# Performance work log

Hardware: AMD Instinct MI355X
Metric: run time of the kernel (lower is better)

Reference implementation:

```python
import jax, jax.numpy as jnp
import numpy as np

B, N, NIN, NH, NOUT = 32, 64, 256, 256, 2
E = N * (N - 1)
BN_EPS = 1e-5


def _xavier(k, fan_in, fan_out):
    return jax.random.normal(k, (fan_in, fan_out), jnp.float32) * np.sqrt(2.0 / (fan_in + fan_out))


def _mlp_params(key, n_in, n_hid, n_out):
    k1, k2 = jax.random.split(key)
    return {
        'w1': _xavier(k1, n_in, n_hid), 'b1': jnp.full((n_hid,), 0.1, jnp.float32),
        'w2': _xavier(k2, n_hid, n_out), 'b2': jnp.full((n_out,), 0.1, jnp.float32),
        'g': jnp.ones((n_out,), jnp.float32), 'beta': jnp.zeros((n_out,), jnp.float32),
    }


def setup_inputs() -> dict:
    key = jax.random.key(0)
    ks = jax.random.split(key, 7)
    inputs = jax.random.normal(ks[0], (B, N, NIN), jnp.float32)
    # fully-connected directed graph w/o self loops: edge e = (send i, recv j), i != j
    idx = np.array([(i, j) for i in range(N) for j in range(N) if i != j], dtype=np.int64)
    rel_send = np.zeros((E, N), np.float32)
    rel_rec = np.zeros((E, N), np.float32)
    rel_send[np.arange(E), idx[:, 0]] = 1.0
    rel_rec[np.arange(E), idx[:, 1]] = 1.0
    out = {'inputs': inputs, 'rel_rec': jnp.asarray(rel_rec), 'rel_send': jnp.asarray(rel_send)}
    for name, (ni, nh, no), k in [('mlp1', (NIN, NH, NH), ks[1]),
                                  ('mlp2', (2 * NH, NH, NH), ks[2]),
                                  ('mlp3', (NH, NH, NH), ks[3]),
                                  ('mlp4', (3 * NH, NH, NH), ks[4])]:
        p = _mlp_params(k, ni, nh, no)
        for pk, pv in p.items():
            out[f'{name}_{pk}'] = pv
    out['fc_w'] = _xavier(ks[5], NH, NOUT)
    out['fc_b'] = jnp.full((NOUT,), 0.1, jnp.float32)
    return out


def _mlp(x, w1, b1, w2, b2, g, beta):
    # Linear -> ELU -> Linear -> ELU -> BatchNorm1d (training-mode batch stats, biased var)
    h = jax.nn.elu(x @ w1 + b1)
    h = jax.nn.elu(h @ w2 + b2)
    mean = h.mean(axis=(0, 1))
    var = h.var(axis=(0, 1))
    return (h - mean) * jax.lax.rsqrt(var + BN_EPS) * g + beta


def reference(inputs, rel_rec, rel_send,
              mlp1_w1, mlp1_b1, mlp1_w2, mlp1_b2, mlp1_g, mlp1_beta,
              mlp2_w1, mlp2_b1, mlp2_w2, mlp2_b2, mlp2_g, mlp2_beta,
              mlp3_w1, mlp3_b1, mlp3_w2, mlp3_b2, mlp3_g, mlp3_beta,
              mlp4_w1, mlp4_b1, mlp4_w2, mlp4_b2, mlp4_g, mlp4_beta,
              fc_w, fc_b):
    x = _mlp(inputs, mlp1_w1, mlp1_b1, mlp1_w2, mlp1_b2, mlp1_g, mlp1_beta)  # [B,N,NH]
    # node2edge: gather sender/receiver node features per edge
    s = jnp.einsum('en,bnh->beh', rel_send, x)
    r = jnp.einsum('en,bnh->beh', rel_rec, x)
    x = jnp.concatenate([s, r], axis=-1)  # [B,E,2*NH]
    x = _mlp(x, mlp2_w1, mlp2_b1, mlp2_w2, mlp2_b2, mlp2_g, mlp2_beta)
    x_skip = x
    # edge2node: scatter-sum incoming edges per node, normalized by N
    inc = jnp.einsum('en,beh->bnh', rel_rec, x) / N
    x = _mlp(inc, mlp3_w1, mlp3_b1, mlp3_w2, mlp3_b2, mlp3_g, mlp3_beta)
    s = jnp.einsum('en,bnh->beh', rel_send, x)
    r = jnp.einsum('en,bnh->beh', rel_rec, x)
    x = jnp.concatenate([s, r, x_skip], axis=-1)  # [B,E,3*NH]
    x = _mlp(x, mlp4_w1, mlp4_b1, mlp4_w2, mlp4_b2, mlp4_g, mlp4_beta)
    return x @ fc_w + fc_b  # [B,E,NOUT]
```

## Files before the change

kernel.cpp:

```cpp
#include <hip/hip_runtime.h>

typedef __bf16 bf16_t;
typedef __bf16 bf16x8 __attribute__((ext_vector_type(8)));
typedef float  f32x4  __attribute__((ext_vector_type(4)));

#define NB    64
#define EB    4032
#define BATCH 32
#define H     256
#define M_EDGE (BATCH*EB)
#define M_NODE (BATCH*NB)
#define T2    4
#define BN_EPS 1e-5f

__device__ __forceinline__ void load_lds16(const void* g, void* l) {
    __builtin_amdgcn_global_load_lds(
        (const __attribute__((address_space(1))) unsigned int*)g,
        (__attribute__((address_space(3))) unsigned int*)l, 16, 0, 0);
}
__device__ __forceinline__ float elu(float v) { return v > 0.f ? v : __expf(v) - 1.f; }

template<bool AF32>
__global__ __launch_bounds__(256, 3)
void fused_mlp(const void* __restrict__ A0v,
               const bf16_t* __restrict__ W1f, const float* __restrict__ b1,
               const bf16_t* __restrict__ W2f, const float* __restrict__ b2,
               bf16_t* __restrict__ out, float* __restrict__ stats)
{
    const int m0 = blockIdx.x * 64;
    const int tid = threadIdx.x, wave = tid >> 6, lane = tid & 63;
    const int l15 = lane & 15, quad = lane >> 4;
    const int row = tid >> 2;
    const int c0 = (tid & 3) * 64;

    __shared__ bf16_t h1s[64 * 264];
    __shared__ float  sred[512];

    sred[tid] = 0.f; sred[256 + tid] = 0.f;

    if (AF32) {
        const float* af = (const float*)A0v + (size_t)(m0 + row) * 256 + c0;
#pragma unroll
        for (int j = 0; j < 8; ++j) {
            float4 lo = *(const float4*)(af + j * 8);
            float4 hi = *(const float4*)(af + j * 8 + 4);
            bf16x8 v;
            v[0]=(bf16_t)lo.x; v[1]=(bf16_t)lo.y; v[2]=(bf16_t)lo.z; v[3]=(bf16_t)lo.w;
            v[4]=(bf16_t)hi.x; v[5]=(bf16_t)hi.y; v[6]=(bf16_t)hi.z; v[7]=(bf16_t)hi.w;
            *(bf16x8*)&h1s[row * 264 + c0 + j * 8] = v;
        }
    } else {
        const bf16_t* src = (const bf16_t*)A0v + (size_t)(m0 + row) * 256 + c0;
#pragma unroll
        for (int j = 0; j < 8; ++j)
            *(bf16x8*)&h1s[row * 264 + c0 + j * 8] = *(const bf16x8*)(src + j * 8);
    }

    const bf16_t* W1W = W1f + (size_t)wave * 16384;
    const bf16_t* W2W = W2f + (size_t)wave * 16384;

    bf16x8 bcur[4], bnxt[4];
#pragma unroll
    for (int u = 0; u < 4; ++u)
        bcur[u] = *(const bf16x8*)(W1W + u * 512 + lane * 8);
    __syncthreads();

    f32x4 acc[4][4];
#pragma unroll
    for (int a = 0; a < 4; ++a)
#pragma unroll
        for (int u = 0; u < 4; ++u) acc[a][u] = (f32x4){0.f, 0.f, 0.f, 0.f};

#pragma unroll
    for (int ks = 0; ks < 8; ++ks) {
        if (ks < 7) {
#pragma unroll
            for (int u = 0; u < 4; ++u)
                bnxt[u] = *(const bf16x8*)(W1W + (ks + 1) * 2048 + u * 512 + lane * 8);
        }
        bf16x8 afr[4];
#pragma unroll
        for (int a = 0; a < 4; ++a)
            afr[a] = *(const bf16x8*)&h1s[(a * 16 + l15) * 264 + ks * 32 + quad * 8];
#pragma unroll
        for (int a = 0; a < 4; ++a)
#pragma unroll
            for (int u = 0; u < 4; ++u)
                acc[a][u] = __builtin_amdgcn_mfma_f32_16x16x32_bf16(afr[a], bcur[u], acc[a][u], 0, 0, 0);
#pragma unroll
        for (int u = 0; u < 4; ++u) bcur[u] = bnxt[u];
    }

#pragma unroll
    for (int u = 0; u < 4; ++u)
        bcur[u] = *(const bf16x8*)(W2W + u * 512 + lane * 8);
    __syncthreads();

#pragma unroll
    for (int u = 0; u < 4; ++u) {
        int   col = wave * 64 + u * 16 + l15;
        float bv  = b1[col];
#pragma unroll
        for (int a = 0; a < 4; ++a)
#pragma unroll
            for (int r = 0; r < 4; ++r)
                h1s[(a * 16 + quad * 4 + r) * 264 + col] = (bf16_t)elu(acc[a][u][r] + bv);
    }
    __syncthreads();

#pragma unroll
    for (int a = 0; a < 4; ++a)
#pragma unroll
        for (int u = 0; u < 4; ++u) acc[a][u] = (f32x4){0.f, 0.f, 0.f, 0.f};
#pragma unroll
    for (int ks = 0; ks < 8; ++ks) {
        if (ks < 7) {
#pragma unroll
            for (int u = 0; u < 4; ++u)
                bnxt[u] = *(const bf16x8*)(W2W + (ks + 1) * 2048 + u * 512 + lane * 8);
        }
        bf16x8 afr[4];
#pragma unroll
        for (int a = 0; a < 4; ++a)
            afr[a] = *(const bf16x8*)&h1s[(a * 16 + l15) * 264 + ks * 32 + quad * 8];
#pragma unroll
        for (int a = 0; a < 4; ++a)
#pragma unroll
            for (int u = 0; u < 4; ++u)
                acc[a][u] = __builtin_amdgcn_mfma_f32_16x16x32_bf16(afr[a], bcur[u], acc[a][u], 0, 0, 0);
#pragma unroll
        for (int u = 0; u < 4; ++u) bcur[u] = bnxt[u];
    }
    __syncthreads();

#pragma unroll
    for (int u = 0; u < 4; ++u) {
        int   col = wave * 64 + u * 16 + l15;
        float bv  = b2[col];
        float s = 0.f, q = 0.f;
#pragma unroll
        for (int a = 0; a < 4; ++a)
#pragma unroll
            for (int r = 0; r < 4; ++r) {
                float v = elu(acc[a][u][r] + bv);
                h1s[(a * 16 + quad * 4 + r) * 264 + col] = (bf16_t)v;
                s += v; q += v * v;
            }
        s += __shfl_xor(s, 16); s += __shfl_xor(s, 32);
        q += __shfl_xor(q, 16); q += __shfl_xor(q, 32);
        if (quad == 0) { atomicAdd(&sred[col], s); atomicAdd(&sred[256 + col], q); }
    }
    __syncthreads();

#pragma unroll
    for (int p = 0; p < 8; ++p) {
        int idx = p * 256 + tid;
        int r = idx >> 5, ch = idx & 31;
        *(uint4*)&out[(size_t)(m0 + r) * H + ch * 8] = *(const uint4*)&h1s[r * 264 + ch * 8];
    }
    atomicAdd(&stats[tid],     sred[tid]);
    atomicAdd(&stats[H + tid], sred[256 + tid]);
}

__global__ __launch_bounds__(256)
void node_gemm(const bf16_t* __restrict__ A, const float* __restrict__ statsIn,
               const float* __restrict__ g, const float* __restrict__ beta, float Mcnt,
               const bf16_t* __restrict__ Wt, const float* __restrict__ bias,
               float* __restrict__ out)
{
    const int m0 = blockIdx.x * 64;
    const int nb = blockIdx.y * 256;
    const int tid = threadIdx.x, wave = tid >> 6, lane = tid & 63;
    const int l15 = lane & 15, quad = lane >> 4;
    const int row = tid >> 2;
    const int cx8 = (((tid & 3) ^ ((tid >> 3) & 3))) * 8;
    const int sl8 = (tid & 3) * 8;
    const int xq8 = (quad ^ ((l15 >> 1) & 3)) * 8;
    __shared__ bf16_t As[64 * 32];
    __shared__ bf16_t Bs[256 * 32];
    __shared__ float  ss[512];

    {
        float mean = statsIn[tid] / Mcnt;
        float var  = statsIn[256 + tid] / Mcnt - mean * mean;
        float scl  = g[tid] * rsqrtf(var + BN_EPS);
        ss[tid]       = scl;
        ss[256 + tid] = beta[tid] - mean * scl;
    }
    __syncthreads();

    f32x4 acc[4][4];
#pragma unroll
    for (int t = 0; t < 4; ++t)
#pragma unroll
        for (int u = 0; u < 4; ++u) acc[t][u] = (f32x4){0.f, 0.f, 0.f, 0.f};

    for (int k0 = 0; k0 < 256; k0 += 32) {
        {
            int kc = k0 + cx8;
            bf16x8 v = *(const bf16x8*)(A + (size_t)(m0 + row) * 256 + kc);
            bf16x8 w;
#pragma unroll
            for (int j = 0; j < 8; ++j)
                w[j] = (bf16_t)((float)v[j] * ss[kc + j] + ss[256 + kc + j]);
            *(bf16x8*)&As[row * 32 + sl8] = w;
        }
#pragma unroll
        for (int p = 0; p < 4; ++p)
            load_lds16(Wt + (size_t)(nb + p * 64 + row) * 256 + k0 + cx8,
                       Bs + (p * 256 + wave * 64) * 8);
        __syncthreads();
        bf16x8 afr[4], bfr[4];
#pragma unroll
        for (int t = 0; t < 4; ++t)
            afr[t] = *(const bf16x8*)&As[(t * 16 + l15) * 32 + xq8];
#pragma unroll
        for (int u = 0; u < 4; ++u)
            bfr[u] = *(const bf16x8*)&Bs[(wave * 64 + u * 16 + l15) * 32 + xq8];
#pragma unroll
        for (int t = 0; t < 4; ++t)
#pragma unroll
            for (int u = 0; u < 4; ++u)
                acc[t][u] = __builtin_amdgcn_mfma_f32_16x16x32_bf16(afr[t], bfr[u], acc[t][u], 0, 0, 0);
        __syncthreads();
    }
#pragma unroll
    for (int u = 0; u < 4; ++u) {
        int col = nb + wave * 64 + u * 16 + l15;
        float bv = bias[col];
#pragma unroll
        for (int t = 0; t < 4; ++t)
#pragma unroll
            for (int r = 0; r < 4; ++r)
                out[(size_t)(m0 + t * 16 + quad * 4 + r) * 512 + col] = acc[t][u][r] + bv;
    }
}

__global__ __launch_bounds__(256, 2)
void m2_kernel(const float* __restrict__ PQ, const bf16_t* __restrict__ W2t,
               const float* __restrict__ b2, bf16_t* __restrict__ out,
               float* __restrict__ stats)
{
    const int tile0 = blockIdx.x * T2;
    const int tid = threadIdx.x, wave = tid >> 6, lane = tid & 63;
    const int l15 = lane & 15, quad = lane >> 4;

    __shared__ bf16_t Abuf[2][64 * 264];
    __shared__ float  sred[512];

    bf16x8 Breg[32];
#pragma unroll
    for (int ks = 0; ks < 8; ++ks)
#pragma unroll
        for (int u = 0; u < 4; ++u) {
            int col = wave * 64 + u * 16 + l15;
            Breg[ks * 4 + u] = *(const bf16x8*)(W2t + (size_t)col * 256 + ks * 32 + quad * 8);
        }
    sred[tid] = 0.f; sred[256 + tid] = 0.f;

    auto computeA = [&](int t, int b) {
        int row = tid >> 2;
        int m = (tile0 + t) * 64 + row;
        int bb = m / EB, e = m - bb * EB;
        int sn = e / (NB - 1), rr = e - sn * (NB - 1);
        int rc = rr + (rr >= sn ? 1 : 0);
        const float* Prow = PQ + (size_t)(bb * NB + sn) * 512;
        const float* Qrow = PQ + (size_t)(bb * NB + rc) * 512 + 256;
        int c0 = (tid & 3) * 64;
#pragma unroll
        for (int j = 0; j < 8; ++j) {
            int c = c0 + j * 8;
            float4 p0 = *(const float4*)(Prow + c);
            float4 p1 = *(const float4*)(Prow + c + 4);
            float4 q0 = *(const float4*)(Qrow + c);
            float4 q1 = *(const float4*)(Qrow + c + 4);
            bf16x8 v;
            v[0]=(bf16_t)elu(p0.x+q0.x); v[1]=(bf16_t)elu(p0.y+q0.y);
            v[2]=(bf16_t)elu(p0.z+q0.z); v[3]=(bf16_t)elu(p0.w+q0.w);
            v[4]=(bf16_t)elu(p1.x+q1.x); v[5]=(bf16_t)elu(p1.y+q1.y);
            v[6]=(bf16_t)elu(p1.z+q1.z); v[7]=(bf16_t)elu(p1.w+q1.w);
            *(bf16x8*)&Abuf[b][row * 264 + c] = v;
        }
    };

    computeA(0, 0);
    __syncthreads();

    for (int t = 0; t < T2; ++t) {
        const int cur = t & 1, nxt = cur ^ 1;
        if (t + 1 < T2) computeA(t + 1, nxt);

        f32x4 acc[4][4];
#pragma unroll
        for (int a = 0; a < 4; ++a)
#pragma unroll
            for (int u = 0; u < 4; ++u) acc[a][u] = (f32x4){0.f, 0.f, 0.f, 0.f};
#pragma unroll
        for (int ks = 0; ks < 8; ++ks) {
            bf16x8 afr[4];
#pragma unroll
            for (int a = 0; a < 4; ++a)
                afr[a] = *(const bf16x8*)&Abuf[cur][(a * 16 + l15) * 264 + ks * 32 + quad * 8];
#pragma unroll
            for (int a = 0; a < 4; ++a)
#pragma unroll
                for (int u = 0; u < 4; ++u)
                    acc[a][u] = __builtin_amdgcn_mfma_f32_16x16x32_bf16(afr[a], Breg[ks * 4 + u], acc[a][u], 0, 0, 0);
        }
        __syncthreads();

#pragma unroll
        for (int u = 0; u < 4; ++u) {
            int   col = wave * 64 + u * 16 + l15;
            float bv  = b2[col];
            float s = 0.f, q = 0.f;
#pragma unroll
            for (int a = 0; a < 4; ++a)
#pragma unroll
                for (int r = 0; r < 4; ++r) {
                    float v = elu(acc[a][u][r] + bv);
                    Abuf[cur][(a * 16 + quad * 4 + r) * 264 + col] = (bf16_t)v;
                    s += v; q += v * v;
                }
            s += __shfl_xor(s, 16); s += __shfl_xor(s, 32);
            q += __shfl_xor(q, 16); q += __shfl_xor(q, 32);
            if (quad == 0) { atomicAdd(&sred[col], s); atomicAdd(&sred[256 + col], q); }
        }
        __syncthreads();

        size_t m0 = (size_t)(tile0 + t) * 64;
#pragma unroll
        for (int p = 0; p < 8; ++p) {
            int idx = p * 256 + tid;
            int r = idx >> 5, ch = idx & 31;
            *(uint4*)&out[(m0 + r) * H + ch * 8] = *(const uint4*)&Abuf[cur][r * 264 + ch * 8];
        }
        __syncthreads();
    }
    atomicAdd(&stats[tid],     sred[tid]);
    atomicAdd(&stats[H + tid], sred[256 + tid]);
}

__global__ __launch_bounds__(256, 3)
void m4_kernel(const bf16_t* __restrict__ h2, const bf16_t* __restrict__ Wskf,
               const float* __restrict__ RS, const bf16_t* __restrict__ W4f,
               const float* __restrict__ b2, bf16_t* __restrict__ out,
               float* __restrict__ stats)
{
    const int m0 = blockIdx.x * 64;
    const int tid = threadIdx.x, wave = tid >> 6, lane = tid & 63;
    const int l15 = lane & 15, quad = lane >> 4;
    const int row = tid >> 2;
    const int c0 = (tid & 3) * 64;

    __shared__ bf16_t h1s[64 * 264];
    __shared__ float  sred[512];
    __shared__ int    sndN[64], rcvN[64];

    sred[tid] = 0.f; sred[256 + tid] = 0.f;
    if (tid < 64) {
        int m = m0 + tid, bb = m / EB, e = m - bb * EB;
        int sn = e / (NB - 1), rr = e - sn * (NB - 1);
        int rc = rr + (rr >= sn ? 1 : 0);
        sndN[tid] = bb * NB + sn;
        rcvN[tid] = bb * NB + rc;
    }

    {
        const bf16_t* src = h2 + (size_t)(m0 + row) * 256;
#pragma unroll
        for (int j = 0; j < 8; ++j) {
            int c = c0 + j * 8;
            *(bf16x8*)&h1s[row * 264 + c] = *(const bf16x8*)(src + c);
        }
    }

    const bf16_t* WskW = Wskf + (size_t)wave * 16384;
    const bf16_t* W4W  = W4f  + (size_t)wave * 16384;

    bf16x8 bcur[4], bnxt[4];
#pragma unroll
    for (int u = 0; u < 4; ++u)
        bcur[u] = *(const bf16x8*)(WskW + u * 512 + lane * 8);
    __syncthreads();

    f32x4 acc[4][4];
#pragma unroll
    for (int a = 0; a < 4; ++a)
#pragma unroll
        for (int r = 0; r < 4; ++r) {
            int ro = a * 16 + quad * 4 + r;
            const float* Srow = RS + (size_t)sndN[ro] * 512;
            const float* Rrow = RS + (size_t)rcvN[ro] * 512 + 256;
#pragma unroll
            for (int u = 0; u < 4; ++u) {
                int co = wave * 64 + u * 16 + l15;
                acc[a][u][r] = Srow[co] + Rrow[co];
            }
        }

#pragma unroll
    for (int ks = 0; ks < 8; ++ks) {
        if (ks < 7) {
#pragma unroll
            for (int u = 0; u < 4; ++u)
                bnxt[u] = *(const bf16x8*)(WskW + (ks + 1) * 2048 + u * 512 + lane * 8);
        }
        bf16x8 afr[4];
#pragma unroll
        for (int a = 0; a < 4; ++a)
            afr[a] = *(const bf16x8*)&h1s[(a * 16 + l15) * 264 + ks * 32 + quad * 8];
#pragma unroll
        for (int a = 0; a < 4; ++a)
#pragma unroll
            for (int u = 0; u < 4; ++u)
                acc[a][u] = __builtin_amdgcn_mfma_f32_16x16x32_bf16(afr[a], bcur[u], acc[a][u], 0, 0, 0);
#pragma unroll
        for (int u = 0; u < 4; ++u) bcur[u] = bnxt[u];
    }

#pragma unroll
    for (int u = 0; u < 4; ++u)
        bcur[u] = *(const bf16x8*)(W4W + u * 512 + lane * 8);
    __syncthreads();

#pragma unroll
    for (int u = 0; u < 4; ++u) {
        int col = wave * 64 + u * 16 + l15;
#pragma unroll
        for (int a = 0; a < 4; ++a)
#pragma unroll
            for (int r = 0; r < 4; ++r)
                h1s[(a * 16 + quad * 4 + r) * 264 + col] = (bf16_t)elu(acc[a][u][r]);
    }
    __syncthreads();

#pragma unroll
    for (int a = 0; a < 4; ++a)
#pragma unroll
        for (int u = 0; u < 4; ++u) acc[a][u] = (f32x4){0.f, 0.f, 0.f, 0.f};
#pragma unroll
    for (int ks = 0; ks < 8; ++ks) {
        if (ks < 7) {
#pragma unroll
            for (int u = 0; u < 4; ++u)
                bnxt[u] = *(const bf16x8*)(W4W + (ks + 1) * 2048 + u * 512 + lane * 8);
        }
        bf16x8 afr[4];
#pragma unroll
        for (int a = 0; a < 4; ++a)
            afr[a] = *(const bf16x8*)&h1s[(a * 16 + l15) * 264 + ks * 32 + quad * 8];
#pragma unroll
        for (int a = 0; a < 4; ++a)
#pragma unroll
            for (int u = 0; u < 4; ++u)
                acc[a][u] = __builtin_amdgcn_mfma_f32_16x16x32_bf16(afr[a], bcur[u], acc[a][u], 0, 0, 0);
#pragma unroll
        for (int u = 0; u < 4; ++u) bcur[u] = bnxt[u];
    }
    __syncthreads();

#pragma unroll
    for (int u = 0; u < 4; ++u) {
        int   col = wave * 64 + u * 16 + l15;
        float bv  = b2[col];
        float s = 0.f, q = 0.f;
#pragma unroll
        for (int a = 0; a < 4; ++a)
#pragma unroll
            for (int r = 0; r < 4; ++r) {
                float v = elu(acc[a][u][r] + bv);
                h1s[(a * 16 + quad * 4 + r) * 264 + col] = (bf16_t)v;
                s += v; q += v * v;
            }
        s += __shfl_xor(s, 16); s += __shfl_xor(s, 32);
        q += __shfl_xor(q, 16); q += __shfl_xor(q, 32);
        if (quad == 0) { atomicAdd(&sred[col], s); atomicAdd(&sred[256 + col], q); }
    }
    __syncthreads();

#pragma unroll
    for (int p = 0; p < 8; ++p) {
        int idx = p * 256 + tid;
        int r = idx >> 5, ch = idx & 31;
        *(uint4*)&out[(size_t)(m0 + r) * H + ch * 8] = *(const uint4*)&h1s[r * 264 + ch * 8];
    }
    atomicAdd(&stats[tid],     sred[tid]);
    atomicAdd(&stats[H + tid], sred[256 + tid]);
}

__global__ void prep(const float* __restrict__ w1a, bf16_t* __restrict__ wt1a,
                     const float* __restrict__ w1b, bf16_t* __restrict__ wt1b,
                     const float* __restrict__ w2b, bf16_t* __restrict__ wt2b,
                     const float* __restrict__ w3a, bf16_t* __restrict__ wt3a,
                     const float* __restrict__ w3b, bf16_t* __restrict__ wt3b,
                     const float* __restrict__ w4b, bf16_t* __restrict__ wt4b,
                     const float* __restrict__ w2a, bf16_t* __restrict__ wtpq,
                     const float* __restrict__ w4a, bf16_t* __restrict__ wtrs,
                     const float* __restrict__ b2a, float* __restrict__ biasPQ,
                     float* __restrict__ stats)
{
    int blk = blockIdx.x, tid = threadIdx.x;
    if (blk < 1536) {
        int grp = blk >> 8, lb = blk & 255;
        int idx = lb * 256 + tid;
        int k = idx >> 8, n = idx & 255;
        if (grp == 2) {
            wt2b[n * 256 + k] = (bf16_t)w2b[idx];
        } else {
            const float* w; bf16_t* wt;
            switch (grp) {
                case 0: w = w1a; wt = wt1a; break;
                case 1: w = w1b; wt = wt1b; break;
                case 3: w = w3a; wt = wt3a; break;
                case 4: w = w3b; wt = wt3b; break;
                default: w = w4b; wt = wt4b; break;
            }
            int wv = n >> 6, u = (n >> 4) & 3, l15 = n & 15;
            int ks = k >> 5, qd = (k >> 3) & 3, j = k & 7;
            wt[wv * 16384 + ks * 2048 + u * 512 + (qd * 16 + l15) * 8 + j] = (bf16_t)w[idx];
        }
    } else if (blk < 2560) {
        int lb = blk - 1536;
        const float* w = (lb < 512) ? w2a : w4a;
        bf16_t* wt = (lb < 512) ? wtpq : wtrs;
        int c = lb & 511, k = tid;
        float v = (c < 256) ? w[k * 256 + c] : w[(256 + k) * 256 + (c - 256)];
        wt[c * 256 + k] = (bf16_t)v;
    } else if (blk == 2560) {
        biasPQ[tid] = b2a[tid];
        biasPQ[256 + tid] = 0.f;
    } else {
        for (int j = 0; j < 8; ++j) stats[j * 256 + tid] = 0.f;
    }
}

__global__ void prep2(const float* __restrict__ w4a, const float* __restrict__ stats2,
                      const float* __restrict__ g2, const float* __restrict__ be2,
                      const float* __restrict__ b4a, bf16_t* __restrict__ wt,
                      float* __restrict__ bias)
{
    __shared__ float sh2s[256];
    int blk = blockIdx.x, tid = threadIdx.x;
    float mean = stats2[tid] / (float)M_EDGE;
    float var  = stats2[256 + tid] / (float)M_EDGE - mean * mean;
    float scl  = g2[tid] * rsqrtf(var + BN_EPS);
    if (blk < 256) {
        int n = blk, k = tid;
        int wv = n >> 6, u = (n >> 4) & 3, l15 = n & 15;
        int ks = k >> 5, qd = (k >> 3) & 3, j = k & 7;
        wt[wv * 16384 + ks * 2048 + u * 512 + (qd * 16 + l15) * 8 + j] =
            (bf16_t)(w4a[(512 + tid) * 256 + blk] * scl);
    } else {
        sh2s[tid] = be2[tid] - mean * scl;
        __syncthreads();
        float acc = 0.f;
        for (int k = 0; k < 256; ++k)
            acc += sh2s[k] * w4a[(512 + k) * 256 + tid];
        bias[tid] = b4a[tid] + acc;
        bias[256 + tid] = 0.f;
    }
}

__global__ void edge2node(const bf16_t* __restrict__ x2, const float* __restrict__ stats2,
                          const float* __restrict__ g2, const float* __restrict__ be2,
                          bf16_t* __restrict__ inc)
{
    int bn = blockIdx.x, bb = bn >> 6, n = bn & 63;
    int g = threadIdx.x >> 5, t = threadIdx.x & 31;
    __shared__ float part[8][256];
    __shared__ float ss[512];
    {
        int c = threadIdx.x;
        float mean = stats2[c] / (float)M_EDGE;
        float var  = stats2[256 + c] / (float)M_EDGE - mean * mean;
        float scl  = g2[c] * rsqrtf(var + BN_EPS);
        ss[c]       = scl;
        ss[256 + c] = be2[c] - mean * scl;
    }
    const bf16_t* base = x2 + (size_t)bb * EB * H;
    float a[8] = {0.f,0.f,0.f,0.f,0.f,0.f,0.f,0.f};
    for (int i = g; i < NB; i += 8) {
        if (i == n) continue;
        int e = i * (NB - 1) + n - (n > i ? 1 : 0);
        bf16x8 v = *(const bf16x8*)&base[(size_t)e * H + t * 8];
#pragma unroll
        for (int j = 0; j < 8; ++j) a[j] += (float)v[j];
    }
#pragma unroll
    for (int j = 0; j < 8; ++j) part[g][t * 8 + j] = a[j];
    __syncthreads();
    int c = threadIdx.x;
    float s = 0.f;
#pragma unroll
    for (int g2i = 0; g2i < 8; ++g2i) s += part[g2i][c];
    inc[(size_t)bn * H + c] = (bf16_t)(s * (1.f / 64.f) * ss[c] + ss[256 + c] * (63.f / 64.f));
}

__global__ void fc_kernel(const bf16_t* __restrict__ x4, const float* __restrict__ stats4,
                          const float* __restrict__ g4, const float* __restrict__ be4,
                          const float* __restrict__ fcw, const float* __restrict__ fcb,
                          float* __restrict__ out)
{
    __shared__ float ss[512];
    {
        int c = threadIdx.x;
        float mean = stats4[c] / (float)M_EDGE;
        float var  = stats4[256 + c] / (float)M_EDGE - mean * mean;
        float scl  = g4[c] * rsqrtf(var + BN_EPS);
        ss[c]       = scl;
        ss[256 + c] = be4[c] - mean * scl;
    }
    __syncthreads();
    int row  = blockIdx.x * 8 + (threadIdx.x >> 5);
    int t    = threadIdx.x & 31;
    bf16x8 v8 = *(const bf16x8*)(x4 + (size_t)row * H + t * 8);
    float s0 = 0.f, s1 = 0.f;
#pragma unroll
    for (int j = 0; j < 8; ++j) {
        int c = t * 8 + j;
        float v = (float)v8[j] * ss[c] + ss[256 + c];
        s0 += v * fcw[c * 2];
        s1 += v * fcw[c * 2 + 1];
    }
#pragma unroll
    for (int off = 16; off; off >>= 1) {
        s0 += __shfl_down(s0, off, 32);
        s1 += __shfl_down(s1, off, 32);
    }
    if (t == 0) {
        out[(size_t)row * 2]     = s0 + fcb[0];
        out[(size_t)row * 2 + 1] = s1 + fcb[1];
    }
}

extern "C" void kernel_launch(void* const* d_in, const int* in_sizes, int n_in,
                              void* d_out, int out_size, void* d_ws, size_t ws_size,
                              hipStream_t stream)
{
    (void)in_sizes; (void)n_in; (void)out_size; (void)ws_size;
    const float* inp = (const float*)d_in[0];
    const float* w1a = (const float*)d_in[3];  const float* b1a = (const float*)d_in[4];
    const float* w1b = (const float*)d_in[5];  const float* b1b = (const float*)d_in[6];
    const float* g1  = (const float*)d_in[7];  const float* be1 = (const float*)d_in[8];
    const float* w2a = (const float*)d_in[9];  const float* b2a = (const float*)d_in[10];
    const float* w2b = (const float*)d_in[11]; const float* b2b = (const float*)d_in[12];
    const float* g2  = (const float*)d_in[13]; const float* be2 = (const float*)d_in[14];
    const float* w3a = (const float*)d_in[15]; const float* b3a = (const float*)d_in[16];
    const float* w3b = (const float*)d_in[17]; const float* b3b = (const float*)d_in[18];
    const float* g3  = (const float*)d_in[19]; const float* be3 = (const float*)d_in[20];
    const float* w4a = (const float*)d_in[21]; const float* b4a = (const float*)d_in[22];
    const float* w4b = (const float*)d_in[23]; const float* b4b = (const float*)d_in[24];
    const float* g4  = (const float*)d_in[25]; const float* be4 = (const float*)d_in[26];
    const float* fcw = (const float*)d_in[27]; const float* fcb = (const float*)d_in[28];

    char* p = (char*)d_ws;
    auto alloc = [&](size_t nbytes) { char* r = p; p += (nbytes + 255) & ~(size_t)255; return r; };

    bf16_t* wt1a = (bf16_t*)alloc(256 * 256 * 2);
    bf16_t* wt1b = (bf16_t*)alloc(256 * 256 * 2);
    bf16_t* wt2b = (bf16_t*)alloc(256 * 256 * 2);
    bf16_t* wt3a = (bf16_t*)alloc(256 * 256 * 2);
    bf16_t* wt3b = (bf16_t*)alloc(256 * 256 * 2);
    bf16_t* wt4b = (bf16_t*)alloc(256 * 256 * 2);
    bf16_t* wtpq = (bf16_t*)alloc(512 * 256 * 2);
    bf16_t* wtrs = (bf16_t*)alloc(512 * 256 * 2);
    bf16_t* wtsk = (bf16_t*)alloc(256 * 256 * 2);
    float*  biasPQ = (float*)alloc(512 * sizeof(float));
    float*  biasRS = (float*)alloc(512 * sizeof(float));
    float*  stats  = (float*)alloc(4 * 512 * sizeof(float));
    bf16_t* x1   = (bf16_t*)alloc((size_t)M_NODE * H * 2);
    bf16_t* incb = (bf16_t*)alloc((size_t)M_NODE * H * 2);
    bf16_t* x3   = (bf16_t*)alloc((size_t)M_NODE * H * 2);
    float*  PQ   = (float*)alloc((size_t)M_NODE * 512 * sizeof(float));
    float*  RS   = (float*)alloc((size_t)M_NODE * 512 * sizeof(float));
    bf16_t* h2   = (bf16_t*)alloc((size_t)M_EDGE * H * 2);
    bf16_t* h4   = (bf16_t*)alloc((size_t)M_EDGE * H * 2);

    prep<<<2562, 256, 0, stream>>>(w1a, wt1a, w1b, wt1b, w2b, wt2b, w3a, wt3a,
                                   w3b, wt3b, w4b, wt4b, w2a, wtpq, w4a, wtrs,
                                   b2a, biasPQ, stats);

    fused_mlp<true ><<<M_NODE / 64, 256, 0, stream>>>(inp, wt1a, b1a, wt1b, b1b, x1, stats + 0);

    { dim3 g(M_NODE / 64, 2);
      node_gemm<<<g, 256, 0, stream>>>(x1, stats + 0, g1, be1, (float)M_NODE, wtpq, biasPQ, PQ); }

    m2_kernel<<<M_EDGE / (64 * T2), 256, 0, stream>>>(PQ, wt2b, b2b, h2, stats + 512);

    edge2node<<<M_NODE, 256, 0, stream>>>(h2, stats + 512, g2, be2, incb);
    fused_mlp<false><<<M_NODE / 64, 256, 0, stream>>>(incb, wt3a, b3a, wt3b, b3b, x3, stats + 1024);

    prep2<<<257, 256, 0, stream>>>(w4a, stats + 512, g2, be2, b4a, wtsk, biasRS);
    { dim3 g(M_NODE / 64, 2);
      node_gemm<<<g, 256, 0, stream>>>(x3, stats + 1024, g3, be3, (float)M_NODE, wtrs, biasRS, RS); }

    m4_kernel<<<M_EDGE / 64, 256, 0, stream>>>(h2, wtsk, RS, wt4b, b4b, h4, stats + 1536);

    fc_kernel<<<M_EDGE / 8, 256, 0, stream>>>(h4, stats + 1536, g4, be4, fcw, fcb, (float*)d_out);
}
```

Baseline: 353.3 us.

## Use async global-to-LDS loads with XOR-swizzled layout in m4_kernel

```diff
diff --git a/kernel.cpp b/kernel.cpp
--- a/kernel.cpp
+++ b/kernel.cpp
@@ -351,38 +351,24 @@
     const int tid = threadIdx.x, wave = tid >> 6, lane = tid & 63;
     const int l15 = lane & 15, quad = lane >> 4;
     const int row = tid >> 2;
-    const int c0 = (tid & 3) * 64;
-
-    __shared__ bf16_t h1s[64 * 264];
+    const int cx8 = (((tid & 3) ^ ((tid >> 3) & 3))) * 8;
+    const int xq8 = (quad ^ ((l15 >> 1) & 3)) * 8;
+
+    __shared__ bf16_t h1s[8 * 2048];
     __shared__ float  sred[512];
-    __shared__ int    sndN[64], rcvN[64];
 
     sred[tid] = 0.f; sred[256 + tid] = 0.f;
-    if (tid < 64) {
-        int m = m0 + tid, bb = m / EB, e = m - bb * EB;
-        int sn = e / (NB - 1), rr = e - sn * (NB - 1);
-        int rc = rr + (rr >= sn ? 1 : 0);
-        sndN[tid] = bb * NB + sn;
-        rcvN[tid] = bb * NB + rc;
-    }
-
-    {
-        const bf16_t* src = h2 + (size_t)(m0 + row) * 256;
-#pragma unroll
-        for (int j = 0; j < 8; ++j) {
-            int c = c0 + j * 8;
-            *(bf16x8*)&h1s[row * 264 + c] = *(const bf16x8*)(src + c);
-        }
-    }
-
-    const bf16_t* WskW = Wskf + (size_t)wave * 16384;
-    const bf16_t* W4W  = W4f  + (size_t)wave * 16384;
-
-    bf16x8 bcur[4], bnxt[4];
-#pragma unroll
-    for (int u = 0; u < 4; ++u)
-        bcur[u] = *(const bf16x8*)(WskW + u * 512 + lane * 8);
-    __syncthreads();
+
+    const int bb  = m0 / EB;
+    const int e0  = m0 - bb * EB;
+    const int sn0 = e0 / (NB - 1);
+    const int rr0 = e0 - sn0 * (NB - 1);
+    const float* RSb = RS + (size_t)(bb * NB) * 512;
+
+#pragma unroll
+    for (int ks = 0; ks < 8; ++ks)
+        load_lds16(h2 + (size_t)(m0 + row) * 256 + ks * 32 + cx8,
+                   h1s + ks * 2048 + wave * 512);
 
     f32x4 acc[4][4];
 #pragma unroll
@@ -390,8 +376,13 @@
 #pragma unroll
         for (int r = 0; r < 4; ++r) {
             int ro = a * 16 + quad * 4 + r;
-            const float* Srow = RS + (size_t)sndN[ro] * 512;
-            const float* Rrow = RS + (size_t)rcvN[ro] * 512 + 256;
+            int t  = rr0 + ro;
+            int wrap = (t >= NB - 1) ? 1 : 0;
+            int sn = sn0 + wrap;
+            int rr = t - (wrap ? (NB - 1) : 0);
+            int rc = rr + (rr >= sn ? 1 : 0);
+            const float* Srow = RSb + (size_t)sn * 512;
+            const float* Rrow = RSb + (size_t)rc * 512 + 256;
 #pragma unroll
             for (int u = 0; u < 4; ++u) {
                 int co = wave * 64 + u * 16 + l15;
@@ -399,6 +390,15 @@
             }
         }
 
+    const bf16_t* WskW = Wskf + (size_t)wave * 16384;
+    const bf16_t* W4W  = W4f  + (size_t)wave * 16384;
+
+    bf16x8 bcur[4], bnxt[4];
+#pragma unroll
+    for (int u = 0; u < 4; ++u)
+        bcur[u] = *(const bf16x8*)(WskW + u * 512 + lane * 8);
+    __syncthreads();
+
 #pragma unroll
     for (int ks = 0; ks < 8; ++ks) {
         if (ks < 7) {
@@ -409,7 +409,7 @@
         bf16x8 afr[4];
 #pragma unroll
         for (int a = 0; a < 4; ++a)
-            afr[a] = *(const bf16x8*)&h1s[(a * 16 + l15) * 264 + ks * 32 + quad * 8];
+            afr[a] = *(const bf16x8*)&h1s[ks * 2048 + (a * 16 + l15) * 32 + xq8];
 #pragma unroll
         for (int a = 0; a < 4; ++a)
 #pragma unroll
@@ -426,12 +426,17 @@
 
 #pragma unroll
     for (int u = 0; u < 4; ++u) {
-        int col = wave * 64 + u * 16 + l15;
-#pragma unroll
-        for (int a = 0; a < 4; ++a)
-#pragma unroll
-            for (int r = 0; r < 4; ++r)
-                h1s[(a * 16 + quad * 4 + r) * 264 + col] = (bf16_t)elu(acc[a][u][r]);
+        const int ks = wave * 2 + (u >> 1);
+        const int qw = (u & 1) * 2 + (l15 >> 3);
+        const int j  = l15 & 7;
+#pragma unroll
+        for (int a = 0; a < 4; ++a)
+#pragma unroll
+            for (int r = 0; r < 4; ++r) {
+                int rw = a * 16 + quad * 4 + r;
+                int qp = qw ^ ((rw >> 1) & 3);
+                h1s[ks * 2048 + rw * 32 + qp * 8 + j] = (bf16_t)elu(acc[a][u][r]);
+            }
     }
     __syncthreads();
 
@@ -449,7 +454,7 @@
         bf16x8 afr[4];
 #pragma unroll
         for (int a = 0; a < 4; ++a)
-            afr[a] = *(const bf16x8*)&h1s[(a * 16 + l15) * 264 + ks * 32 + quad * 8];
+            afr[a] = *(const bf16x8*)&h1s[ks * 2048 + (a * 16 + l15) * 32 + xq8];
 #pragma unroll
         for (int a = 0; a < 4; ++a)
 #pragma unroll
@@ -462,15 +467,20 @@
 
 #pragma unroll
     for (int u = 0; u < 4; ++u) {
-        int   col = wave * 64 + u * 16 + l15;
-        float bv  = b2[col];
+        const int col = wave * 64 + u * 16 + l15;
+        const float bv = b2[col];
+        const int ks = wave * 2 + (u >> 1);
+        const int qw = (u & 1) * 2 + (l15 >> 3);
+        const int j  = l15 & 7;
         float s = 0.f, q = 0.f;
 #pragma unroll
         for (int a = 0; a < 4; ++a)
 #pragma unroll
             for (int r = 0; r < 4; ++r) {
                 float v = elu(acc[a][u][r] + bv);
-                h1s[(a * 16 + quad * 4 + r) * 264 + col] = (bf16_t)v;
+                int rw = a * 16 + quad * 4 + r;
+                int qp = qw ^ ((rw >> 1) & 3);
+                h1s[ks * 2048 + rw * 32 + qp * 8 + j] = (bf16_t)v;
                 s += v; q += v * v;
             }
         s += __shfl_xor(s, 16); s += __shfl_xor(s, 32);
@@ -483,7 +493,8 @@
     for (int p = 0; p < 8; ++p) {
         int idx = p * 256 + tid;
         int r = idx >> 5, ch = idx & 31;
-        *(uint4*)&out[(size_t)(m0 + r) * H + ch * 8] = *(const uint4*)&h1s[r * 264 + ch * 8];
+        *(uint4*)&out[(size_t)(m0 + r) * H + ch * 8] =
+            *(const uint4*)&h1s[(ch >> 2) * 2048 + r * 32 + (((ch & 3) ^ ((r >> 1) & 3)) * 8)];
     }
     atomicAdd(&stats[tid],     sred[tid]);
     atomicAdd(&stats[H + tid], sred[256 + tid]);
```

New measurement: 352.5 us. No clear change (-0.2%).
